# Kernel tuning notes

Hardware: AMD Instinct MI355X
Metric: run time of the kernel (lower is better)

Reference implementation:

```python
import jax, jax.numpy as jnp
import numpy as np

N_VARS = 512
K = 32
B = 192
LOG2PI = 1.8378770664093453


def setup_inputs() -> dict:
    key = jax.random.key(0)
    k1, k2, k3, k4, k5 = jax.random.split(key, 5)
    X = jax.random.normal(k1, (B, N_VARS), dtype=jnp.float32)
    # one-hot cluster assignment matrix C: [n_vars, k]
    assign = jax.random.randint(k2, (N_VARS,), 0, K)
    C = jax.nn.one_hot(assign, K, dtype=jnp.float32)
    # cluster-level adjacency G: [k, k], binary
    G = (jax.random.uniform(k3, (K, K)) < 0.3).astype(jnp.float32)
    W = jax.random.normal(k4, (N_VARS, N_VARS), dtype=jnp.float32) / np.sqrt(N_VARS).astype(np.float32)
    b = jax.random.normal(k5, (N_VARS,), dtype=jnp.float32) * 0.01
    sigma = jnp.array([0.1], dtype=jnp.float32)
    rho = jnp.array([0.99], dtype=jnp.float32)
    return dict(X=X, C=C, G=G, W=W, b=b, sigma=sigma, rho=rho)


def reference(X, C, G, W, b, sigma, rho):
    n = X.shape[1]
    # expand cluster adjacency to variable-level mask: [n, n]
    G_expand = C @ G @ C.T
    # MaskedLinear: F.linear(X, W * mask, b)
    mean = X @ (W * G_expand).T + b  # [B, n]
    # cluster-structured covariance: sigma^2 * ((1-rho) I + rho * C C^T)
    M = C @ C.T  # same-cluster indicator (incl. diagonal)
    Cov = (sigma[0] ** 2) * ((1.0 - rho[0]) * jnp.eye(n, dtype=X.dtype) + rho[0] * M)
    L = jnp.linalg.cholesky(Cov)
    # torch MVN broadcasting: value [B,1,n] vs loc [B,n] -> log_prob [B,B]
    diff = X[:, None, :] - mean[None, :, :]  # [B, B, n]
    nb = diff.shape[0] * diff.shape[1]
    rhs = diff.reshape(nb, n).T  # [n, B*B]
    y = jax.scipy.linalg.solve_triangular(L, rhs, lower=True)  # [n, B*B]
    maha = jnp.sum(y * y, axis=0)  # [B*B]
    logdet = 2.0 * jnp.sum(jnp.log(jnp.diagonal(L)))
    logp = -0.5 * (maha + logdet + n * LOG2PI)
    return logp.mean()
```

## Files before the change

### kernel.cpp

```cpp
#include <hip/hip_runtime.h>
#include <math.h>

#define NV 512
#define KC 32
#define NB 192
#define LOG2PI 1.8378770664093453f

typedef __attribute__((ext_vector_type(8))) short short8;
typedef __attribute__((ext_vector_type(4))) float float4v;

#define WS_SM    0
#define WS_GV    6144
#define WS_STATS 12400
#define WS_P     27000
#define WS_ASG   27040
#define WS_XBF   27552
#define WS_WBF   76704

static __device__ inline ushort f2bf(float f) {
    uint u = __float_as_uint(f);
    uint r = (u + 0x7fffu + ((u >> 16) & 1u)) >> 16;
    return (ushort)r;
}

__global__ __launch_bounds__(256) void prep_kernel(
    const float* __restrict__ X, const float* __restrict__ C,
    const float* __restrict__ G, const float* __restrict__ W,
    const float* __restrict__ bias, const float* __restrict__ sigma,
    const float* __restrict__ rho, float* __restrict__ wsF, int* __restrict__ wsI)
{
    const int bid = blockIdx.x, tid = threadIdx.x;
    __shared__ int asg[NV];
    __shared__ float Gs[KC * KC];
    __shared__ float smrows[8][KC];
    __shared__ float redw[4];

    for (int n = tid; n < NV; n += 256) {
        const float* row = C + n * KC;
        float a = 0.f;
        #pragma unroll
        for (int c = 0; c < KC; ++c) a += row[c] * (float)c;
        asg[n] = (int)(a + 0.5f);
    }

    if (bid < 24) {
        __syncthreads();
        ushort* xbf = (ushort*)(wsF + WS_XBF);
        const int base = bid * 8 * NV;
        #pragma unroll
        for (int p = 0; p < 4; ++p) {
            const int off = base + tid * 4 + p * 1024;
            const float4 f = *(const float4*)(X + off);
            ushort4 o;
            o.x = f2bf(f.x); o.y = f2bf(f.y); o.z = f2bf(f.z); o.w = f2bf(f.w);
            *(ushort4*)(xbf + off) = o;
        }
    } else if (bid < 88) {
        for (int l = tid; l < KC * KC; l += 256) Gs[l] = G[l];
        __syncthreads();
        ushort* wbf = (ushort*)(wsF + WS_WBF);
        const int i0 = (bid - 24) * 8;
        #pragma unroll
        for (int p = 0; p < 4; ++p) {
            const int l = tid * 4 + p * 1024;
            const int ir = i0 + (l >> 9), k = l & 511;
            const float* grow = Gs + asg[ir] * KC;
            const float4 f = *(const float4*)(W + ir * NV + k);
            ushort4 o;
            o.x = f2bf(f.x * grow[asg[k]]);
            o.y = f2bf(f.y * grow[asg[k + 1]]);
            o.z = f2bf(f.z * grow[asg[k + 2]]);
            o.w = f2bf(f.w * grow[asg[k + 3]]);
            *(ushort4*)(wbf + ir * NV + k) = o;
        }
    } else if (bid < 112) {
        for (int l = tid; l < 8 * KC; l += 256) ((float*)smrows)[l] = 0.f;
        if (tid < 4) redw[tid] = 0.f;
        __syncthreads();
        const int sb = bid - 88, row0 = sb * 8;
        const int c0 = tid * 2;
        const int ca = asg[c0], cb = asg[c0 + 1];
        float u0 = 0.f, u1 = 0.f, xx = 0.f;
        #pragma unroll
        for (int r = 0; r < 8; ++r) {
            const float2 xv = *(const float2*)(X + (row0 + r) * NV + c0);
            u0 += xv.x; u1 += xv.y;
            xx += xv.x * xv.x + xv.y * xv.y;
            atomicAdd(&smrows[r][ca], xv.x);
            atomicAdd(&smrows[r][cb], xv.y);
        }
        for (int off = 32; off; off >>= 1) xx += __shfl_down(xx, off, 64);
        if ((tid & 63) == 0) redw[tid >> 6] = xx;
        __syncthreads();
        float* slice = wsF + WS_STATS + sb * 608;
        slice[c0] = u0; slice[c0 + 1] = u1;
        if (tid < KC) {
            float s1 = 0.f, s2 = 0.f;
            #pragma unroll
            for (int r = 0; r < 8; ++r) { const float s = smrows[r][tid]; s1 += s; s2 += s * s; }
            slice[512 + tid] = s1;
            slice[544 + tid] = s2;
        }
        if (tid == 0) slice[576] = redw[0] + redw[1] + redw[2] + redw[3];
    } else {
        __shared__ int cnt[KC];
        __shared__ float ldred[KC];
        if (tid < KC) cnt[tid] = 0;
        __syncthreads();
        for (int n = tid; n < NV; n += 256) {
            atomicAdd(&cnt[asg[n]], 1);
            wsI[WS_ASG + n] = asg[n];
        }
        for (int l = tid; l < NB * KC; l += 256) wsF[WS_SM + l] = 0.f;
        __syncthreads();
        const float s2v = sigma[0] * sigma[0], rh = rho[0];
        const float av = s2v * (1.f - rh), bv = s2v * rh;
        if (tid < KC) {
            const int nc = cnt[tid];
            wsF[WS_P + tid] = bv / (av * (av + bv * (float)nc));
            ldred[tid] = (float)(nc - 1) * logf(av) + logf(av + bv * (float)nc);
        }
        __syncthreads();
        if (tid == 0) {
            float ld = 0.f;
            for (int c = 0; c < KC; ++c) ld += ldred[c];
            wsF[WS_P + 32] = ld;
        }
    }
}

__global__ __launch_bounds__(256) void gemm_kernel(
    const float* __restrict__ bias, float* __restrict__ wsF, const int* __restrict__ wsI)
{
    const int bid = blockIdx.x, tid = threadIdx.x;
    const int blk_b = bid >> 3, blk_i = bid & 7;
    const int b0 = blk_b * 16, i0blk = blk_i * 64;
    const int w = tid >> 6, lane = tid & 63;
    const int m = lane & 15, q = lane >> 4;
    const int i0w = i0blk + w * 16;

    __shared__ float smL[16 * KC];
    __shared__ float varr[64];
    __shared__ int asgc[64];
    __shared__ float mmred[4];
    for (int l = tid; l < 16 * KC; l += 256) smL[l] = 0.f;
    if (tid < 64) { varr[tid] = 0.f; asgc[tid] = wsI[WS_ASG + i0blk + tid]; }
    if (tid < 4) mmred[tid] = 0.f;

    const ushort* xbf = (const ushort*)(wsF + WS_XBF);
    const ushort* wbf = (const ushort*)(wsF + WS_WBF);
    const short8* ap = (const short8*)(xbf + (b0 + m) * NV + q * 8);
    const short8* bp = (const short8*)(wbf + (i0w + m) * NV + q * 8);
    float4v acc = {0.f, 0.f, 0.f, 0.f};
    #pragma unroll
    for (int s = 0; s < 16; ++s) {
        const short8 a = ap[s * 4];
        const short8 b = bp[s * 4];
        acc = __builtin_amdgcn_mfma_f32_16x16x32_bf16(a, b, acc, 0, 0, 0);
    }
    __syncthreads();

    const int col = i0w + m;
    const float bv = bias[col];
    const int ca = asgc[w * 16 + m];
    float vsum = 0.f, mml = 0.f;
    #pragma unroll
    for (int r = 0; r < 4; ++r) {
        const float val = acc[r] + bv;
        vsum += val; mml += val * val;
        atomicAdd(&smL[(q * 4 + r) * KC + ca], val);
    }
    atomicAdd(&varr[w * 16 + m], vsum);
    for (int off = 32; off; off >>= 1) mml += __shfl_down(mml, off, 64);
    if (lane == 0) mmred[w] = mml;
    __syncthreads();

    float* smG = wsF + WS_SM;
    for (int l = tid; l < 16 * KC; l += 256)
        atomicAdd(&smG[(b0 + (l >> 5)) * KC + (l & 31)], smL[l]);
    float* slice = wsF + WS_GV + bid * 65;
    if (tid < 64) slice[tid] = varr[tid];
    if (tid == 0) slice[64] = mmred[0] + mmred[1] + mmred[2] + mmred[3];
}

__global__ __launch_bounds__(256) void finalize_kernel(
    const float* __restrict__ sigma, const float* __restrict__ rho,
    const float* __restrict__ wsF, float* __restrict__ out)
{
    const int tid = threadIdx.x;
    __shared__ float SM1s[KC], SM2s[KC];
    __shared__ float accs[4];
    if (tid < KC) { SM1s[tid] = 0.f; SM2s[tid] = 0.f; }
    if (tid < 4) accs[tid] = 0.f;
    __syncthreads();
    const float* sm = wsF + WS_SM;
    const float* gv = wsF + WS_GV;
    const float* st = wsF + WS_STATS;

    {
        const int c = tid & 31, r0 = tid >> 5;
        float s1 = 0.f, s2 = 0.f;
        #pragma unroll
        for (int j = 0; j < 24; ++j) {
            const float s = sm[(r0 + 8 * j) * KC + c];
            s1 += s; s2 += s * s;
        }
        atomicAdd(&SM1s[c], s1);
        atomicAdd(&SM2s[c], s2);
    }
    {
        float cr = 0.f;
        #pragma unroll
        for (int h = 0; h < 2; ++h) {
            const int i = tid + h * 256;
            float u = 0.f;
            #pragma unroll
            for (int sb = 0; sb < 24; ++sb) u += st[sb * 608 + i];
            float v = 0.f;
            const int blk_i = i >> 6, loc = i & 63;
            #pragma unroll
            for (int bb = 0; bb < 12; ++bb) v += gv[(bb * 8 + blk_i) * 65 + loc];
            cr += u * v;
        }
        for (int off = 32; off; off >>= 1) cr += __shfl_down(cr, off, 64);
        if ((tid & 63) == 0) atomicAdd(&accs[2], cr);
    }
    {
        float mm = (tid < 96) ? gv[tid * 65 + 64] : 0.f;
        for (int off = 32; off; off >>= 1) mm += __shfl_down(mm, off, 64);
        if ((tid & 63) == 0) atomicAdd(&accs[0], mm);
    }
    {
        float xx = (tid < 24) ? st[tid * 608 + 576] : 0.f;
        for (int off = 32; off; off >>= 1) xx += __shfl_down(xx, off, 64);
        if ((tid & 63) == 0) atomicAdd(&accs[1], xx);
    }
    __syncthreads();
    {
        float qv = 0.f;
        if (tid < KC) {
            float s1 = 0.f, s2 = 0.f;
            #pragma unroll
            for (int sb = 0; sb < 24; ++sb) {
                s1 += st[sb * 608 + 512 + tid];
                s2 += st[sb * 608 + 544 + tid];
            }
            const float coef = wsF[WS_P + tid];
            qv = coef * (s2 * (1.f / NB) + SM2s[tid] * (1.f / NB)
                         - 2.f * s1 * SM1s[tid] * (1.f / ((float)NB * (float)NB)));
        }
        for (int off = 32; off; off >>= 1) qv += __shfl_down(qv, off, 64);
        if (tid == 0) atomicAdd(&accs[3], qv);
    }
    __syncthreads();
    if (tid == 0) {
        const float s2v = sigma[0] * sigma[0], rh = rho[0];
        const float av = s2v * (1.f - rh);
        const float meanD2 = accs[1] * (1.f / NB) + accs[0] * (1.f / NB)
                           - 2.f * accs[2] / ((float)NB * (float)NB);
        const float maha = meanD2 / av - accs[3];
        out[0] = -0.5f * (maha + wsF[WS_P + 32] + (float)NV * LOG2PI);
    }
}

extern "C" void kernel_launch(void* const* d_in, const int* in_sizes, int n_in,
                              void* d_out, int out_size, void* d_ws, size_t ws_size,
                              hipStream_t stream) {
    const float* X     = (const float*)d_in[0];
    const float* C     = (const float*)d_in[1];
    const float* G     = (const float*)d_in[2];
    const float* W     = (const float*)d_in[3];
    const float* b     = (const float*)d_in[4];
    const float* sigma = (const float*)d_in[5];
    const float* rho   = (const float*)d_in[6];
    float* wsF = (float*)d_ws;
    int*   wsI = (int*)d_ws;
    float* out = (float*)d_out;

    hipLaunchKernelGGL(prep_kernel, dim3(113), dim3(256), 0, stream,
                       X, C, G, W, b, sigma, rho, wsF, wsI);
    hipLaunchKernelGGL(gemm_kernel, dim3(96), dim3(256), 0, stream,
                       b, wsF, wsI);
    hipLaunchKernelGGL(finalize_kernel, dim3(1), dim3(256), 0, stream,
                       sigma, rho, wsF, out);
}
```

Measured before the change: 86.87 us.

## Fuse prep and GEMM into one kernel with in-register bf16 conversion and masking

```diff
diff --git a/kernel.cpp b/kernel.cpp
--- a/kernel.cpp
+++ b/kernel.cpp
@@ -8,129 +8,23 @@
 
 typedef __attribute__((ext_vector_type(8))) short short8;
 typedef __attribute__((ext_vector_type(4))) float float4v;
-
-#define WS_SM    0
-#define WS_GV    6144
-#define WS_STATS 12400
-#define WS_P     27000
-#define WS_ASG   27040
-#define WS_XBF   27552
-#define WS_WBF   76704
-
-static __device__ inline ushort f2bf(float f) {
-    uint u = __float_as_uint(f);
-    uint r = (u + 0x7fffu + ((u >> 16) & 1u)) >> 16;
-    return (ushort)r;
-}
-
-__global__ __launch_bounds__(256) void prep_kernel(
+typedef __attribute__((ext_vector_type(4))) int int4v;
+
+#define WS_GS 0
+#define GS_STRIDE 592
+#define WS_ST 56832
+#define ST_STRIDE 580
+#define WS_P 63792
+
+static __device__ inline uint pkbf(uint lo, uint hi) {
+    return ((hi + 0x8000u) & 0xffff0000u) | ((lo + 0x8000u) >> 16);
+}
+
+__global__ __launch_bounds__(256) void mega_kernel(
     const float* __restrict__ X, const float* __restrict__ C,
     const float* __restrict__ G, const float* __restrict__ W,
     const float* __restrict__ bias, const float* __restrict__ sigma,
-    const float* __restrict__ rho, float* __restrict__ wsF, int* __restrict__ wsI)
-{
-    const int bid = blockIdx.x, tid = threadIdx.x;
-    __shared__ int asg[NV];
-    __shared__ float Gs[KC * KC];
-    __shared__ float smrows[8][KC];
-    __shared__ float redw[4];
-
-    for (int n = tid; n < NV; n += 256) {
-        const float* row = C + n * KC;
-        float a = 0.f;
-        #pragma unroll
-        for (int c = 0; c < KC; ++c) a += row[c] * (float)c;
-        asg[n] = (int)(a + 0.5f);
-    }
-
-    if (bid < 24) {
-        __syncthreads();
-        ushort* xbf = (ushort*)(wsF + WS_XBF);
-        const int base = bid * 8 * NV;
-        #pragma unroll
-        for (int p = 0; p < 4; ++p) {
-            const int off = base + tid * 4 + p * 1024;
-            const float4 f = *(const float4*)(X + off);
-            ushort4 o;
-            o.x = f2bf(f.x); o.y = f2bf(f.y); o.z = f2bf(f.z); o.w = f2bf(f.w);
-            *(ushort4*)(xbf + off) = o;
-        }
-    } else if (bid < 88) {
-        for (int l = tid; l < KC * KC; l += 256) Gs[l] = G[l];
-        __syncthreads();
-        ushort* wbf = (ushort*)(wsF + WS_WBF);
-        const int i0 = (bid - 24) * 8;
-        #pragma unroll
-        for (int p = 0; p < 4; ++p) {
-            const int l = tid * 4 + p * 1024;
-            const int ir = i0 + (l >> 9), k = l & 511;
-            const float* grow = Gs + asg[ir] * KC;
-            const float4 f = *(const float4*)(W + ir * NV + k);
-            ushort4 o;
-            o.x = f2bf(f.x * grow[asg[k]]);
-            o.y = f2bf(f.y * grow[asg[k + 1]]);
-            o.z = f2bf(f.z * grow[asg[k + 2]]);
-            o.w = f2bf(f.w * grow[asg[k + 3]]);
-            *(ushort4*)(wbf + ir * NV + k) = o;
-        }
-    } else if (bid < 112) {
-        for (int l = tid; l < 8 * KC; l += 256) ((float*)smrows)[l] = 0.f;
-        if (tid < 4) redw[tid] = 0.f;
-        __syncthreads();
-        const int sb = bid - 88, row0 = sb * 8;
-        const int c0 = tid * 2;
-        const int ca = asg[c0], cb = asg[c0 + 1];
-        float u0 = 0.f, u1 = 0.f, xx = 0.f;
-        #pragma unroll
-        for (int r = 0; r < 8; ++r) {
-            const float2 xv = *(const float2*)(X + (row0 + r) * NV + c0);
-            u0 += xv.x; u1 += xv.y;
-            xx += xv.x * xv.x + xv.y * xv.y;
-            atomicAdd(&smrows[r][ca], xv.x);
-            atomicAdd(&smrows[r][cb], xv.y);
-        }
-        for (int off = 32; off; off >>= 1) xx += __shfl_down(xx, off, 64);
-        if ((tid & 63) == 0) redw[tid >> 6] = xx;
-        __syncthreads();
-        float* slice = wsF + WS_STATS + sb * 608;
-        slice[c0] = u0; slice[c0 + 1] = u1;
-        if (tid < KC) {
-            float s1 = 0.f, s2 = 0.f;
-            #pragma unroll
-            for (int r = 0; r < 8; ++r) { const float s = smrows[r][tid]; s1 += s; s2 += s * s; }
-            slice[512 + tid] = s1;
-            slice[544 + tid] = s2;
-        }
-        if (tid == 0) slice[576] = redw[0] + redw[1] + redw[2] + redw[3];
-    } else {
-        __shared__ int cnt[KC];
-        __shared__ float ldred[KC];
-        if (tid < KC) cnt[tid] = 0;
-        __syncthreads();
-        for (int n = tid; n < NV; n += 256) {
-            atomicAdd(&cnt[asg[n]], 1);
-            wsI[WS_ASG + n] = asg[n];
-        }
-        for (int l = tid; l < NB * KC; l += 256) wsF[WS_SM + l] = 0.f;
-        __syncthreads();
-        const float s2v = sigma[0] * sigma[0], rh = rho[0];
-        const float av = s2v * (1.f - rh), bv = s2v * rh;
-        if (tid < KC) {
-            const int nc = cnt[tid];
-            wsF[WS_P + tid] = bv / (av * (av + bv * (float)nc));
-            ldred[tid] = (float)(nc - 1) * logf(av) + logf(av + bv * (float)nc);
-        }
-        __syncthreads();
-        if (tid == 0) {
-            float ld = 0.f;
-            for (int c = 0; c < KC; ++c) ld += ldred[c];
-            wsF[WS_P + 32] = ld;
-        }
-    }
-}
-
-__global__ __launch_bounds__(256) void gemm_kernel(
-    const float* __restrict__ bias, float* __restrict__ wsF, const int* __restrict__ wsI)
+    const float* __restrict__ rho, float* __restrict__ wsF)
 {
     const int bid = blockIdx.x, tid = threadIdx.x;
     const int blk_b = bid >> 3, blk_i = bid & 7;
@@ -139,51 +33,166 @@
     const int m = lane & 15, q = lane >> 4;
     const int i0w = i0blk + w * 16;
 
+    __shared__ int asg[NV];
+    __shared__ float Gs[KC * KC];
+    __shared__ uint Gbits[KC];
+    __shared__ unsigned long long kmask[KC][8];
     __shared__ float smL[16 * KC];
     __shared__ float varr[64];
-    __shared__ int asgc[64];
     __shared__ float mmred[4];
+    __shared__ float smrows[16][KC];
+    __shared__ int cnt[KC];
+    __shared__ float ldred[KC];
+
+    {
+        const int n0 = tid * 2;
+        #pragma unroll
+        for (int h = 0; h < 2; ++h) {
+            const int n = n0 + h;
+            const float* row = C + n * KC;
+            float a = 0.f;
+            #pragma unroll
+            for (int c4 = 0; c4 < 8; ++c4) {
+                const float4 f = *(const float4*)(row + c4 * 4);
+                a += f.x * (float)(c4 * 4) + f.y * (float)(c4 * 4 + 1)
+                   + f.z * (float)(c4 * 4 + 2) + f.w * (float)(c4 * 4 + 3);
+            }
+            asg[n] = (int)(a + 0.5f);
+        }
+    }
+    for (int l = tid; l < KC * KC; l += 256) Gs[l] = G[l];
     for (int l = tid; l < 16 * KC; l += 256) smL[l] = 0.f;
-    if (tid < 64) { varr[tid] = 0.f; asgc[tid] = wsI[WS_ASG + i0blk + tid]; }
-    if (tid < 4) mmred[tid] = 0.f;
-
-    const ushort* xbf = (const ushort*)(wsF + WS_XBF);
-    const ushort* wbf = (const ushort*)(wsF + WS_WBF);
-    const short8* ap = (const short8*)(xbf + (b0 + m) * NV + q * 8);
-    const short8* bp = (const short8*)(wbf + (i0w + m) * NV + q * 8);
+    if (tid < 64) varr[tid] = 0.f;
+    __syncthreads();
+    if (tid < KC) {
+        uint bits = 0;
+        #pragma unroll
+        for (int c2 = 0; c2 < KC; ++c2)
+            bits |= (Gs[tid * KC + c2] > 0.5f ? 1u : 0u) << c2;
+        Gbits[tid] = bits;
+    }
+    __syncthreads();
+    #pragma unroll
+    for (int gi = 0; gi < 2; ++gi) {
+        const int g = w * 2 + gi;
+        const int a = asg[g * 64 + lane];
+        #pragma unroll
+        for (int c1 = 0; c1 < KC; ++c1) {
+            const unsigned long long bm = __ballot((Gbits[c1] >> a) & 1u);
+            if (lane == c1) kmask[c1][g] = bm;
+        }
+    }
+    __syncthreads();
+
+    const int carow = asg[i0w + m];
+    unsigned long long rm[8];
+    #pragma unroll
+    for (int g = 0; g < 8; ++g) rm[g] = kmask[carow][g];
+    const float* aRow = X + (b0 + m) * NV;
+    const float* bRow = W + (i0w + m) * NV;
+    const int q8 = q * 8;
     float4v acc = {0.f, 0.f, 0.f, 0.f};
     #pragma unroll
     for (int s = 0; s < 16; ++s) {
-        const short8 a = ap[s * 4];
-        const short8 b = bp[s * 4];
-        acc = __builtin_amdgcn_mfma_f32_16x16x32_bf16(a, b, acc, 0, 0, 0);
-    }
-    __syncthreads();
+        const int k0 = q8 + s * 32;
+        const float4 a0 = *(const float4*)(aRow + k0);
+        const float4 a1 = *(const float4*)(aRow + k0 + 4);
+        const float4 w0 = *(const float4*)(bRow + k0);
+        const float4 w1 = *(const float4*)(bRow + k0 + 4);
+        const uint bits = (uint)(rm[s >> 1] >> (q8 + ((s & 1) << 5))) & 0xffu;
+        const uint b0u = (bits & 1u)   ? __float_as_uint(w0.x) : 0u;
+        const uint b1u = (bits & 2u)   ? __float_as_uint(w0.y) : 0u;
+        const uint b2u = (bits & 4u)   ? __float_as_uint(w0.z) : 0u;
+        const uint b3u = (bits & 8u)   ? __float_as_uint(w0.w) : 0u;
+        const uint b4u = (bits & 16u)  ? __float_as_uint(w1.x) : 0u;
+        const uint b5u = (bits & 32u)  ? __float_as_uint(w1.y) : 0u;
+        const uint b6u = (bits & 64u)  ? __float_as_uint(w1.z) : 0u;
+        const uint b7u = (bits & 128u) ? __float_as_uint(w1.w) : 0u;
+        int4v ai, bi;
+        ai.x = (int)pkbf(__float_as_uint(a0.x), __float_as_uint(a0.y));
+        ai.y = (int)pkbf(__float_as_uint(a0.z), __float_as_uint(a0.w));
+        ai.z = (int)pkbf(__float_as_uint(a1.x), __float_as_uint(a1.y));
+        ai.w = (int)pkbf(__float_as_uint(a1.z), __float_as_uint(a1.w));
+        bi.x = (int)pkbf(b0u, b1u);
+        bi.y = (int)pkbf(b2u, b3u);
+        bi.z = (int)pkbf(b4u, b5u);
+        bi.w = (int)pkbf(b6u, b7u);
+        acc = __builtin_amdgcn_mfma_f32_16x16x32_bf16(
+            __builtin_bit_cast(short8, ai), __builtin_bit_cast(short8, bi), acc, 0, 0, 0);
+    }
 
     const int col = i0w + m;
     const float bv = bias[col];
-    const int ca = asgc[w * 16 + m];
     float vsum = 0.f, mml = 0.f;
     #pragma unroll
     for (int r = 0; r < 4; ++r) {
         const float val = acc[r] + bv;
         vsum += val; mml += val * val;
-        atomicAdd(&smL[(q * 4 + r) * KC + ca], val);
+        atomicAdd(&smL[(q * 4 + r) * KC + carow], val);
     }
     atomicAdd(&varr[w * 16 + m], vsum);
     for (int off = 32; off; off >>= 1) mml += __shfl_down(mml, off, 64);
     if (lane == 0) mmred[w] = mml;
     __syncthreads();
-
-    float* smG = wsF + WS_SM;
-    for (int l = tid; l < 16 * KC; l += 256)
-        atomicAdd(&smG[(b0 + (l >> 5)) * KC + (l & 31)], smL[l]);
-    float* slice = wsF + WS_GV + bid * 65;
-    if (tid < 64) slice[tid] = varr[tid];
-    if (tid == 0) slice[64] = mmred[0] + mmred[1] + mmred[2] + mmred[3];
-}
-
-__global__ __launch_bounds__(256) void finalize_kernel(
+    {
+        float* slice = wsF + WS_GS + bid * GS_STRIDE;
+        for (int l = tid; l < 16 * KC; l += 256) slice[l] = smL[l];
+        if (tid < 64) slice[512 + tid] = varr[tid];
+        if (tid == 0) slice[576] = mmred[0] + mmred[1] + mmred[2] + mmred[3];
+    }
+
+    if (blk_i == 0) {
+        __syncthreads();
+        for (int l = tid; l < 16 * KC; l += 256) ((float*)smrows)[l] = 0.f;
+        __syncthreads();
+        const int c0 = tid * 2;
+        const int ca = asg[c0], cb = asg[c0 + 1];
+        float u0 = 0.f, u1 = 0.f, xx = 0.f;
+        #pragma unroll
+        for (int r = 0; r < 16; ++r) {
+            const float2 xv = *(const float2*)(X + (b0 + r) * NV + c0);
+            u0 += xv.x; u1 += xv.y;
+            xx += xv.x * xv.x + xv.y * xv.y;
+            atomicAdd(&smrows[r][ca], xv.x);
+            atomicAdd(&smrows[r][cb], xv.y);
+        }
+        for (int off = 32; off; off >>= 1) xx += __shfl_down(xx, off, 64);
+        if ((tid & 63) == 0) mmred[tid >> 6] = xx;
+        __syncthreads();
+        float* st = wsF + WS_ST + blk_b * ST_STRIDE;
+        st[c0] = u0; st[c0 + 1] = u1;
+        if (tid < KC) {
+            float s1 = 0.f, s2 = 0.f;
+            #pragma unroll
+            for (int r = 0; r < 16; ++r) { const float s = smrows[r][tid]; s1 += s; s2 += s * s; }
+            st[512 + tid] = s1;
+            st[544 + tid] = s2;
+        }
+        if (tid == 0) st[576] = mmred[0] + mmred[1] + mmred[2] + mmred[3];
+    }
+
+    if (bid == 0) {
+        if (tid < KC) cnt[tid] = 0;
+        __syncthreads();
+        for (int n = tid; n < NV; n += 256) atomicAdd(&cnt[asg[n]], 1);
+        __syncthreads();
+        const float s2v = sigma[0] * sigma[0], rh = rho[0];
+        const float av = s2v * (1.f - rh), bvv = s2v * rh;
+        if (tid < KC) {
+            const int nc = cnt[tid];
+            wsF[WS_P + tid] = bvv / (av * (av + bvv * (float)nc));
+            ldred[tid] = (float)(nc - 1) * logf(av) + logf(av + bvv * (float)nc);
+        }
+        __syncthreads();
+        if (tid == 0) {
+            float ld = 0.f;
+            for (int c = 0; c < KC; ++c) ld += ldred[c];
+            wsF[WS_P + 32] = ld;
+        }
+    }
+}
+
+__global__ __launch_bounds__(512) void finalize_kernel(
     const float* __restrict__ sigma, const float* __restrict__ rho,
     const float* __restrict__ wsF, float* __restrict__ out)
 {
@@ -193,45 +202,40 @@
     if (tid < KC) { SM1s[tid] = 0.f; SM2s[tid] = 0.f; }
     if (tid < 4) accs[tid] = 0.f;
     __syncthreads();
-    const float* sm = wsF + WS_SM;
-    const float* gv = wsF + WS_GV;
-    const float* st = wsF + WS_STATS;
-
-    {
-        const int c = tid & 31, r0 = tid >> 5;
+    const float* gs = wsF + WS_GS;
+    const float* st = wsF + WS_ST;
+
+    {
+        const int c = tid & 31, g = tid >> 5;
         float s1 = 0.f, s2 = 0.f;
-        #pragma unroll
-        for (int j = 0; j < 24; ++j) {
-            const float s = sm[(r0 + 8 * j) * KC + c];
+        for (int bb = g; bb < NB; bb += 16) {
+            const float* p = gs + ((bb >> 4) * 8) * GS_STRIDE + (bb & 15) * KC + c;
+            float s = 0.f;
+            #pragma unroll
+            for (int ib = 0; ib < 8; ++ib) s += p[ib * GS_STRIDE];
             s1 += s; s2 += s * s;
         }
         atomicAdd(&SM1s[c], s1);
         atomicAdd(&SM2s[c], s2);
     }
     {
-        float cr = 0.f;
-        #pragma unroll
-        for (int h = 0; h < 2; ++h) {
-            const int i = tid + h * 256;
-            float u = 0.f;
-            #pragma unroll
-            for (int sb = 0; sb < 24; ++sb) u += st[sb * 608 + i];
-            float v = 0.f;
-            const int blk_i = i >> 6, loc = i & 63;
-            #pragma unroll
-            for (int bb = 0; bb < 12; ++bb) v += gv[(bb * 8 + blk_i) * 65 + loc];
-            cr += u * v;
-        }
+        float v = 0.f, u = 0.f;
+        #pragma unroll
+        for (int bb = 0; bb < 12; ++bb)
+            v += gs[(bb * 8 + (tid >> 6)) * GS_STRIDE + 512 + (tid & 63)];
+        #pragma unroll
+        for (int sb = 0; sb < 12; ++sb) u += st[sb * ST_STRIDE + tid];
+        float cr = u * v;
         for (int off = 32; off; off >>= 1) cr += __shfl_down(cr, off, 64);
         if ((tid & 63) == 0) atomicAdd(&accs[2], cr);
     }
     {
-        float mm = (tid < 96) ? gv[tid * 65 + 64] : 0.f;
+        float mm = (tid < 96) ? gs[tid * GS_STRIDE + 576] : 0.f;
         for (int off = 32; off; off >>= 1) mm += __shfl_down(mm, off, 64);
         if ((tid & 63) == 0) atomicAdd(&accs[0], mm);
     }
     {
-        float xx = (tid < 24) ? st[tid * 608 + 576] : 0.f;
+        float xx = (tid < 12) ? st[tid * ST_STRIDE + 576] : 0.f;
         for (int off = 32; off; off >>= 1) xx += __shfl_down(xx, off, 64);
         if ((tid & 63) == 0) atomicAdd(&accs[1], xx);
     }
@@ -241,9 +245,9 @@
         if (tid < KC) {
             float s1 = 0.f, s2 = 0.f;
             #pragma unroll
-            for (int sb = 0; sb < 24; ++sb) {
-                s1 += st[sb * 608 + 512 + tid];
-                s2 += st[sb * 608 + 544 + tid];
+            for (int sb = 0; sb < 12; ++sb) {
+                s1 += st[sb * ST_STRIDE + 512 + tid];
+                s2 += st[sb * ST_STRIDE + 544 + tid];
             }
             const float coef = wsF[WS_P + tid];
             qv = coef * (s2 * (1.f / NB) + SM2s[tid] * (1.f / NB)
@@ -274,13 +278,10 @@
     const float* sigma = (const float*)d_in[5];
     const float* rho   = (const float*)d_in[6];
     float* wsF = (float*)d_ws;
-    int*   wsI = (int*)d_ws;
     float* out = (float*)d_out;
 
-    hipLaunchKernelGGL(prep_kernel, dim3(113), dim3(256), 0, stream,
-                       X, C, G, W, b, sigma, rho, wsF, wsI);
-    hipLaunchKernelGGL(gemm_kernel, dim3(96), dim3(256), 0, stream,
-                       b, wsF, wsI);
-    hipLaunchKernelGGL(finalize_kernel, dim3(1), dim3(256), 0, stream,
+    hipLaunchKernelGGL(mega_kernel, dim3(96), dim3(256), 0, stream,
+                       X, C, G, W, b, sigma, rho, wsF);
+    hipLaunchKernelGGL(finalize_kernel, dim3(1), dim3(512), 0, stream,
                        sigma, rho, wsF, out);
 }
```

Measured after the change: 106.7 us. 1.23x slower.
